# Optimization experiments

Measured on AMD Instinct MI355X. Metric: run time of the kernel, lower is better.

The kernel has to match this reference:

```python
import jax, jax.numpy as jnp
import numpy as np

B, N, H, E, OBS, A, AFF, EFF = 2, 50000, 64, 1_000_000, 128, 18, 512, 256


def setup_inputs() -> dict:
    key = jax.random.key(0)
    ks = jax.random.split(key, 20)
    s = 0.05  # small init to keep gates/tanh unsaturated
    return {
        "obs": jax.random.normal(ks[0], (B, OBS), jnp.float32),
        "state": jax.random.normal(ks[1], (B, N, H), jnp.float32) * 0.1,
        "W_in": jax.random.normal(ks[2], (OBS, H), jnp.float32) * s,
        "b_in": jnp.zeros((H,), jnp.float32),
        "W_msg": jax.random.normal(ks[3], (H, H), jnp.float32) * s,
        "W_gate": jax.random.normal(ks[4], (2 * H, H), jnp.float32) * s,
        "b_gate": jnp.zeros((H,), jnp.float32),
        "W_cand": jax.random.normal(ks[5], (2 * H, H), jnp.float32) * s,
        "b_cand": jnp.zeros((H,), jnp.float32),
        "W_dec": jax.random.normal(ks[6], (H, H), jnp.float32) * s,
        "b_dec": jnp.zeros((H,), jnp.float32),
        "W_mean": jax.random.normal(ks[7], (H, A), jnp.float32) * s,
        "b_mean": jnp.zeros((A,), jnp.float32),
        "W_ls": jax.random.normal(ks[8], (H, A), jnp.float32) * s,
        "b_ls": jnp.zeros((A,), jnp.float32),
        "src_index": jax.random.randint(ks[9], (E,), 0, N),
        "dst_index": jax.random.randint(ks[10], (E,), 0, N),
        "afferent_idx": jax.random.randint(ks[11], (AFF,), 0, N),
        "efferent_idx": jax.random.randint(ks[12], (EFF,), 0, N),
    }


def reference(obs, state, W_in, b_in, W_msg, W_gate, b_gate, W_cand, b_cand,
              W_dec, b_dec, W_mean, b_mean, W_ls, b_ls,
              src_index, dst_index, afferent_idx, efferent_idx):
    # inject obs projection into afferent node slots
    projected = obs @ W_in + b_in                                   # [B, H]
    injected = jnp.zeros_like(state).at[:, afferent_idx, :].set(projected[:, None, :])
    # gather-project-scatter message passing over the edge list
    src_msgs = state[:, src_index, :] @ W_msg                       # [B, E, H]
    messages = jnp.zeros_like(state).at[:, dst_index, :].add(src_msgs)
    # GRU-style gated update
    combined = messages + injected
    gate_in = jnp.concatenate([state, combined], axis=-1)           # [B, N, 2H]
    z = jax.nn.sigmoid(gate_in @ W_gate + b_gate)
    cand = jnp.tanh(gate_in @ W_cand + b_cand)
    next_state = (1.0 - z) * state + z * cand
    # mean-pool readout over efferent nodes, then policy heads
    readout = next_state[:, efferent_idx, :].mean(axis=1)           # [B, H]
    decoded = jnp.tanh(readout @ W_dec + b_dec)
    mean = decoded @ W_mean + b_mean
    log_std = jnp.clip(decoded @ W_ls + b_ls, -5.0, 2.0)
    return mean, log_std, next_state
```

## Files before the change

kernel.cpp:

```cpp
#include <hip/hip_runtime.h>
#include <hip/hip_bf16.h>

constexpr int kN   = 50000;
constexpr int kH   = 64;
constexpr int kB   = 2;
constexpr int kE   = 1000000;
constexpr int kObs = 128;
constexpr int kA   = 18;
constexpr int kAff = 512;
constexpr int kEff = 256;
constexpr int kNH  = kN * kH;
constexpr int kOutOff = 2 * kB * kA;
constexpr int kRanges = 8;
constexpr int kNr  = kN / kRanges;
constexpr int kChunks = 64;
constexpr int kEc  = kE / kChunks;
constexpr int kHistB = kRanges * kChunks;
constexpr int kPackBlocks = (kNH + 8191) / 8192;
constexpr int kWprepBlocks = 20;
constexpr int kScanB = (kN + 255) / 256;

typedef __attribute__((ext_vector_type(8))) short short8_t;
typedef __attribute__((ext_vector_type(4))) float f32x4_t;

__device__ __forceinline__ float ldf(const void* p, int i, int f32) {
  if (f32) return ((const float*)p)[i];
  unsigned short u = ((const unsigned short*)p)[i];
  union { unsigned int x; float f; } v; v.x = ((unsigned int)u) << 16; return v.f;
}
__device__ __forceinline__ void stf(void* p, int i, float val, int f32) {
  if (f32) ((float*)p)[i] = val;
  else ((__hip_bfloat16*)p)[i] = __float2bfloat16(val);
}
__device__ __forceinline__ float lo16(unsigned int w) {
  union { unsigned int i; float f; } v; v.i = w << 16; return v.f;
}
__device__ __forceinline__ float hi16(unsigned int w) {
  union { unsigned int i; float f; } v; v.i = w & 0xffff0000u; return v.f;
}
__device__ __forceinline__ float b2f(unsigned short u) {
  union { unsigned int i; float f; } v; v.i = ((unsigned int)u) << 16; return v.f;
}
__device__ __forceinline__ unsigned int f2b(float f) {
  union { float f; unsigned int u; } v; v.f = f;
  unsigned int r = v.u + 0x7fffu + ((v.u >> 16) & 1u);
  return r >> 16;
}
__device__ __forceinline__ float fsig(float x) {
  return __builtin_amdgcn_rcpf(1.f + __expf(-x));
}
__device__ __forceinline__ float ftanh(float x) {
  return 1.f - 2.f * __builtin_amdgcn_rcpf(__expf(2.f * x) + 1.f);
}
__device__ __forceinline__ int detect64(const unsigned short* wprobe, int t) {
  int hits = 0;
  for (int k = 0; k < 4; ++k) {
    unsigned short u = wprobe[(t * 4 + k) * 2];
    int e = (u >> 7) & 0xFF;
    if ((u & 0x7FFFu) != 0 && e >= 108 && e <= 128) hits++;
  }
  for (int off = 32; off; off >>= 1) hits += __shfl_down(hits, off);
  return (hits < 128) ? 1 : 0;
}

extern "C" __global__ __launch_bounds__(1024) void k_prep(
    const unsigned short* __restrict__ wprobe,
    const void* __restrict__ obs,
    const void* __restrict__ W_in,
    const void* __restrict__ b_in,
    const int* __restrict__ aff_idx,
    const int* __restrict__ dst,
    const void* __restrict__ W_msg,
    const void* __restrict__ W_gate,
    const void* __restrict__ W_cand,
    int* __restrict__ dflag,
    int* __restrict__ flags,
    float* __restrict__ projected,
    int* __restrict__ deg_c,
    unsigned short* __restrict__ wt) {
  __shared__ int sdeg[kNr];
  int t = threadIdx.x, b = blockIdx.x;
  if (b == 0) {
    __shared__ int sflag;
    if (t < 64) { int f = detect64(wprobe, t); if (t == 0) { sflag = f; dflag[0] = f; } }
    for (int i = t; i < kN; i += 1024) flags[i] = 0;
    __syncthreads();
    int f32 = sflag;
    if (t < kAff) flags[aff_idx[t]] = 1;
    if (t < kB * kH) {
      int bb = t >> 6, h = t & 63;
      float acc = ldf(b_in, h, f32);
      for (int o = 0; o < kObs; ++o)
        acc += ldf(obs, bb * kObs + o, f32) * ldf(W_in, o * kH + h, f32);
      projected[t] = acc;
    }
  } else if (b <= kHistB) {
    int h = b - 1, r = h & 7, c = h >> 3;
    int r0 = r * kNr;
    for (int i = t; i < kNr; i += 1024) sdeg[i] = 0;
    __syncthreads();
    int end = (c + 1) * kEc;
    for (int e = c * kEc + t; e < end; e += 1024) {
      unsigned rel = (unsigned)(dst[e] - r0);
      if (rel < (unsigned)kNr) atomicAdd(&sdeg[rel], 1);
    }
    __syncthreads();
    for (int i = t; i < kNr; i += 1024) deg_c[c * kN + r0 + i] = sdeg[i];
  } else {
    __shared__ int sflag;
    if (t < 64) { int f = detect64(wprobe, t); if (t == 0) sflag = f; }
    __syncthreads();
    int f32 = sflag;
    int i = (b - 1 - kHistB) * 1024 + t;
    if (i < 4096) {
      int n = i >> 6, k = i & 63;
      wt[i] = (unsigned short)f2b(ldf(W_msg, k * 64 + n, f32));
    } else if (i < 12288) {
      int j = i - 4096; int n = j >> 7, k = j & 127;
      wt[i] = (unsigned short)f2b(ldf(W_gate, k * 64 + n, f32));
    } else if (i < 20480) {
      int j = i - 12288; int n = j >> 7, k = j & 127;
      wt[i] = (unsigned short)f2b(ldf(W_cand, k * 64 + n, f32));
    }
  }
}

extern "C" __global__ void k_scan1(const int* __restrict__ deg_c,
                                   int* __restrict__ row_off,
                                   int* __restrict__ partials) {
  __shared__ int sd[256];
  int t = threadIdx.x;
  int n = blockIdx.x * 256 + t;
  int s = 0;
  if (n < kN) {
    for (int c = 0; c < kChunks; ++c) s += deg_c[c * kN + n];
  }
  sd[t] = s;
  __syncthreads();
  for (int off = 1; off < 256; off <<= 1) {
    int v = (t >= off) ? sd[t - off] : 0;
    __syncthreads();
    sd[t] += v;
    __syncthreads();
  }
  int excl = sd[t] - s;
  if (t == 255) partials[blockIdx.x] = sd[255];
  if (n < kN) row_off[n] = excl;
}

extern "C" __global__ void k_scan3(int* __restrict__ row_off,
                                   const int* __restrict__ partials,
                                   int* __restrict__ deg_c) {
  __shared__ int sd[256];
  int t = threadIdx.x;
  int s = 0;
  for (int j = t; j < (int)blockIdx.x; j += 256) s += partials[j];
  sd[t] = s;
  __syncthreads();
  for (int off = 128; off; off >>= 1) {
    if (t < off) sd[t] += sd[t + off];
    __syncthreads();
  }
  int base = sd[0];
  int n = blockIdx.x * 256 + t;
  if (n < kN) {
    int v = row_off[n] + base;
    row_off[n] = v;
    int run = v;
#pragma unroll 8
    for (int c = 0; c < kChunks; ++c) {
      int d = deg_c[c * kN + n];
      deg_c[c * kN + n] = run;
      run += d;
    }
  }
  if (blockIdx.x == 0 && t == 0) row_off[kN] = kE;
}

extern "C" __global__ __launch_bounds__(1024) void k_scatter(
    const int* __restrict__ src,
    const int* __restrict__ dst,
    const int* __restrict__ chunk_base,
    int* __restrict__ sorted_src,
    const unsigned short* __restrict__ wprobe,
    const void* __restrict__ state,
    unsigned int* __restrict__ pack) {
  __shared__ int scur[kNr];
  int t = threadIdx.x;
  if (blockIdx.x < kHistB) {
    int r = blockIdx.x & 7, c = blockIdx.x >> 3;
    int r0 = r * kNr;
    for (int i = t; i < kNr; i += 1024) scur[i] = chunk_base[c * kN + r0 + i];
    __syncthreads();
    int end = (c + 1) * kEc;
    for (int e = c * kEc + t; e < end; e += 1024) {
      unsigned rel = (unsigned)(dst[e] - r0);
      if (rel < (unsigned)kNr) {
        int pos = atomicAdd(&scur[rel], 1);
        sorted_src[pos] = src[e];
      }
    }
  } else {
    __shared__ int sflag;
    if (t < 64) { int f = detect64(wprobe, t); if (t == 0) sflag = f; }
    __syncthreads();
    int f32 = sflag;
    int i = (blockIdx.x - kHistB) * 8192 + t * 8;
    if (i < kNH) {
      uint4 o0, o1;
      if (!f32) {
        uint4 a = *(const uint4*)((const unsigned short*)state + i);
        uint4 c4 = *(const uint4*)((const unsigned short*)state + kNH + i);
        o0.x = (a.x & 0xffffu) | (c4.x << 16);
        o0.y = (a.x >> 16)     | (c4.x & 0xffff0000u);
        o0.z = (a.y & 0xffffu) | (c4.y << 16);
        o0.w = (a.y >> 16)     | (c4.y & 0xffff0000u);
        o1.x = (a.z & 0xffffu) | (c4.z << 16);
        o1.y = (a.z >> 16)     | (c4.z & 0xffff0000u);
        o1.z = (a.w & 0xffffu) | (c4.w << 16);
        o1.w = (a.w >> 16)     | (c4.w & 0xffff0000u);
      } else {
        const float* sf = (const float*)state;
        unsigned int w[8];
#pragma unroll
        for (int k = 0; k < 8; ++k)
          w[k] = f2b(sf[i + k]) | (f2b(sf[kNH + i + k]) << 16);
        o0 = make_uint4(w[0], w[1], w[2], w[3]);
        o1 = make_uint4(w[4], w[5], w[6], w[7]);
      }
      *(uint4*)&pack[i] = o0;
      *(uint4*)&pack[i + 4] = o1;
    }
  }
}

extern "C" __global__ __launch_bounds__(256) void k_gather(
    const unsigned int* __restrict__ pack,
    const int* __restrict__ row_off,
    const int* __restrict__ sorted_src,
    unsigned int* __restrict__ agg) {
  int wave = threadIdx.x >> 6, lane = threadIdx.x & 63;
  int n = blockIdx.x * 4 + wave;
  if (n >= kN) return;
  int s  = row_off[n];
  int en = row_off[n + 1];
  int g = lane >> 4, col = lane & 15;
  const uint4* pk4 = (const uint4*)pack;
  float a0x = 0.f, a0y = 0.f, a0z = 0.f, a0w = 0.f;
  float a1x = 0.f, a1y = 0.f, a1z = 0.f, a1w = 0.f;
  for (int e = s; e < en; e += 8) {
#pragma unroll
    for (int h = 0; h < 2; ++h) {
      int ee = e + h * 4 + g;
      int idx = sorted_src[min(ee, en - 1)];
      uint4 wv = pk4[idx * 16 + col];
      if (ee >= en) { wv.x = 0u; wv.y = 0u; wv.z = 0u; wv.w = 0u; }
      a0x += lo16(wv.x); a1x += hi16(wv.x);
      a0y += lo16(wv.y); a1y += hi16(wv.y);
      a0z += lo16(wv.z); a1z += hi16(wv.z);
      a0w += lo16(wv.w); a1w += hi16(wv.w);
    }
  }
  a0x += __shfl_xor(a0x, 16); a0x += __shfl_xor(a0x, 32);
  a0y += __shfl_xor(a0y, 16); a0y += __shfl_xor(a0y, 32);
  a0z += __shfl_xor(a0z, 16); a0z += __shfl_xor(a0z, 32);
  a0w += __shfl_xor(a0w, 16); a0w += __shfl_xor(a0w, 32);
  a1x += __shfl_xor(a1x, 16); a1x += __shfl_xor(a1x, 32);
  a1y += __shfl_xor(a1y, 16); a1y += __shfl_xor(a1y, 32);
  a1z += __shfl_xor(a1z, 16); a1z += __shfl_xor(a1z, 32);
  a1w += __shfl_xor(a1w, 16); a1w += __shfl_xor(a1w, 32);
  if (g == 0) {
    uint4 o;
    o.x = f2b(a0x) | (f2b(a1x) << 16);
    o.y = f2b(a0y) | (f2b(a1y) << 16);
    o.z = f2b(a0z) | (f2b(a1z) << 16);
    o.w = f2b(a0w) | (f2b(a1w) << 16);
    ((uint4*)agg)[n * 16 + col] = o;
  }
}

extern "C" __global__ __launch_bounds__(256) void k_update(
    const unsigned int* __restrict__ pk,
    const unsigned short* __restrict__ wt,
    const void* __restrict__ b_gate,
    const void* __restrict__ b_cand,
    const unsigned int* __restrict__ agg,
    const int* __restrict__ flags,
    const float* __restrict__ projected,
    const int* __restrict__ dflag,
    void* __restrict__ out) {
  __shared__ uint4 lx4[1088];
  unsigned short* lx = (unsigned short*)lx4;
  int f32 = dflag[0];
  int t = threadIdx.x;
  int w = t >> 6, lane = t & 63;
  int q = lane >> 4, l15 = lane & 15;
  int rowb = w * 16;
  int nd0 = blockIdx.x * 32;
  int ndw = nd0 + w * 8;

  const uint4* pk4 = (const uint4*)pk;
  const uint4* ag4 = (const uint4*)agg;
  for (int j = lane; j < 128; j += 64) {
    int ndl = j >> 4, c4 = j & 15;
    int ndg = min(ndw + ndl, kN - 1);
    uint4 pv = pk4[ndg * 16 + c4];
    uint4 av = ag4[ndg * 16 + c4];
    int r0 = rowb + 2 * ndl;
    *(uint2*)&lx[r0 * 136 + c4 * 4] =
        make_uint2((pv.x & 0xffffu) | (pv.y << 16), (pv.z & 0xffffu) | (pv.w << 16));
    *(uint2*)&lx[(r0 + 1) * 136 + c4 * 4] =
        make_uint2((pv.x >> 16) | (pv.y & 0xffff0000u), (pv.z >> 16) | (pv.w & 0xffff0000u));
    *(uint2*)&lx[r0 * 136 + 64 + c4 * 4] =
        make_uint2((av.x & 0xffffu) | (av.y << 16), (av.z & 0xffffu) | (av.w << 16));
    *(uint2*)&lx[(r0 + 1) * 136 + 64 + c4 * 4] =
        make_uint2((av.x >> 16) | (av.y & 0xffff0000u), (av.z >> 16) | (av.w & 0xffff0000u));
  }

  const unsigned short* wm = wt;
  const unsigned short* wg = wt + 4096;
  const unsigned short* wc = wt + 12288;

  short8_t a0 = *(const short8_t*)&lx[(rowb + l15) * 136 + 64 + q * 8];
  short8_t a1 = *(const short8_t*)&lx[(rowb + l15) * 136 + 96 + q * 8];
  f32x4_t msgc[4];
#pragma unroll
  for (int ct = 0; ct < 4; ++ct) {
    f32x4_t acc = {0.f, 0.f, 0.f, 0.f};
    short8_t b0 = *(const short8_t*)&wm[(ct * 16 + l15) * 64 + q * 8];
    short8_t b1 = *(const short8_t*)&wm[(ct * 16 + l15) * 64 + 32 + q * 8];
    acc = __builtin_amdgcn_mfma_f32_16x16x32_bf16(a0, b0, acc, 0, 0, 0);
    acc = __builtin_amdgcn_mfma_f32_16x16x32_bf16(a1, b1, acc, 0, 0, 0);
    msgc[ct] = acc;
  }
  int nA = ndw + q * 2, nB = nA + 1;
  int flA = (nA < kN) ? flags[nA] : 0;
  int flB = (nB < kN) ? flags[nB] : 0;
#pragma unroll
  for (int ct = 0; ct < 4; ++ct) {
    int col = ct * 16 + l15;
    float pj0 = projected[col], pj1 = projected[64 + col];
#pragma unroll
    for (int r = 0; r < 4; ++r) {
      int row = rowb + q * 4 + r;
      int fl = (r < 2) ? flA : flB;
      float inj = fl ? ((row & 1) ? pj1 : pj0) : 0.f;
      lx[row * 136 + 64 + col] = (unsigned short)f2b(msgc[ct][r] + inj);
    }
  }

  short8_t xa[4];
#pragma unroll
  for (int ks = 0; ks < 4; ++ks)
    xa[ks] = *(const short8_t*)&lx[(rowb + l15) * 136 + ks * 32 + q * 8];
  float ps[16];
#pragma unroll
  for (int ct = 0; ct < 4; ++ct)
#pragma unroll
    for (int rp = 0; rp < 2; ++rp) {
      int row = rowb + q * 4 + 2 * rp;
      ps[ct * 4 + rp * 2 + 0] = b2f(lx[row * 136 + ct * 16 + l15]);
      ps[ct * 4 + rp * 2 + 1] = b2f(lx[(row + 1) * 136 + ct * 16 + l15]);
    }
  float* soutw = (float*)((char*)lx4 + w * 4352);
#pragma unroll
  for (int ct = 0; ct < 4; ++ct) {
    f32x4_t accg = {0.f, 0.f, 0.f, 0.f}, accc = {0.f, 0.f, 0.f, 0.f};
#pragma unroll
    for (int ks = 0; ks < 4; ++ks) {
      short8_t bg = *(const short8_t*)&wg[(ct * 16 + l15) * 128 + ks * 32 + q * 8];
      short8_t bc = *(const short8_t*)&wc[(ct * 16 + l15) * 128 + ks * 32 + q * 8];
      accg = __builtin_amdgcn_mfma_f32_16x16x32_bf16(xa[ks], bg, accg, 0, 0, 0);
      accc = __builtin_amdgcn_mfma_f32_16x16x32_bf16(xa[ks], bc, accc, 0, 0, 0);
    }
    int col = ct * 16 + l15;
    float bgv = ldf(b_gate, col, f32), bcv = ldf(b_cand, col, f32);
#pragma unroll
    for (int rp = 0; rp < 2; ++rp) {
      int r = q * 4 + 2 * rp;
      float z0 = fsig(accg[2 * rp] + bgv);
      float c0 = ftanh(accc[2 * rp] + bcv);
      soutw[r * 64 + col] = (1.f - z0) * ps[ct * 4 + rp * 2 + 0] + z0 * c0;
      float z1 = fsig(accg[2 * rp + 1] + bgv);
      float c1 = ftanh(accc[2 * rp + 1] + bcv);
      soutw[(r + 1) * 64 + col] = (1.f - z1) * ps[ct * 4 + rp * 2 + 1] + z1 * c1;
    }
  }
  __syncthreads();

  int nvalid = min(32, kN - nd0) * 64;
  if (f32) {
    float* po = (float*)out + kOutOff;
#pragma unroll
    for (int p = 0; p < 2; ++p)
      for (int j = t * 4; j < nvalid; j += 1024) {
        int ndl = j >> 6, c = j & 63;
        int wv = ndl >> 3, r = ((ndl & 7) << 1) + p;
        float4 v = *(float4*)((char*)lx4 + wv * 4352 + r * 256 + c * 4);
        *(float4*)(po + p * kNH + nd0 * 64 + j) = v;
      }
  } else {
    unsigned short* po = (unsigned short*)out + kOutOff;
#pragma unroll
    for (int p = 0; p < 2; ++p)
      for (int j = t * 8; j < nvalid; j += 2048) {
        int ndl = j >> 6, c = j & 63;
        int wv = ndl >> 3, r = ((ndl & 7) << 1) + p;
        const char* base = (const char*)lx4 + wv * 4352 + r * 256 + c * 4;
        float4 v0 = *(const float4*)base;
        float4 v1 = *(const float4*)(base + 16);
        uint4 o;
        o.x = f2b(v0.x) | (f2b(v0.y) << 16);
        o.y = f2b(v0.z) | (f2b(v0.w) << 16);
        o.z = f2b(v1.x) | (f2b(v1.y) << 16);
        o.w = f2b(v1.z) | (f2b(v1.w) << 16);
        *(uint4*)(po + p * kNH + nd0 * 64 + j) = o;
      }
  }
}

extern "C" __global__ void k_readout(const void* __restrict__ W_dec,
                                     const void* __restrict__ b_dec,
                                     const void* __restrict__ W_mean,
                                     const void* __restrict__ b_mean,
                                     const void* __restrict__ W_ls,
                                     const void* __restrict__ b_ls,
                                     const int* __restrict__ eff_idx,
                                     const int* __restrict__ dflag,
                                     void* __restrict__ out) {
  __shared__ float part[8][64];
  __shared__ float ro[128], dec[128];
  int f32 = dflag[0];
  int t = threadIdx.x;
  int wv = t >> 6, lane = t & 63;
  int b = wv >> 2, g = wv & 3;
  float acc = 0.f;
#pragma unroll 4
  for (int i = 0; i < 64; ++i) {
    int n = eff_idx[g * 64 + i];
    acc += ldf(out, kOutOff + b * kNH + n * 64 + lane, f32);
  }
  part[wv][lane] = acc;
  __syncthreads();
  if (t < 128) {
    int bb = t >> 6, h = t & 63;
    float s = part[bb * 4 + 0][h] + part[bb * 4 + 1][h] +
              part[bb * 4 + 2][h] + part[bb * 4 + 3][h];
    ro[t] = s * (1.f / kEff);
  }
  __syncthreads();
  if (t < 128) {
    int bb = t >> 6, h = t & 63;
    float d = ldf(b_dec, h, f32);
    for (int k = 0; k < 64; ++k) d += ro[bb * 64 + k] * ldf(W_dec, k * 64 + h, f32);
    dec[t] = tanhf(d);
  }
  __syncthreads();
  if (t < kB * kA) {
    int bb = t / kA, a = t % kA;
    float m = ldf(b_mean, a, f32), l = ldf(b_ls, a, f32);
    for (int k = 0; k < 64; ++k) {
      float dv = dec[bb * 64 + k];
      m += dv * ldf(W_mean, k * kA + a, f32);
      l += dv * ldf(W_ls, k * kA + a, f32);
    }
    l = fminf(fmaxf(l, -5.f), 2.f);
    stf(out, t, m, f32);
    stf(out, kB * kA + t, l, f32);
  }
}

extern "C" void kernel_launch(void* const* d_in, const int* in_sizes, int n_in,
                              void* d_out, int out_size, void* d_ws, size_t ws_size,
                              hipStream_t stream) {
  (void)in_sizes; (void)n_in; (void)out_size; (void)ws_size;
  const void* obs    = d_in[0];
  const void* state  = d_in[1];
  const void* W_in   = d_in[2];
  const void* b_in   = d_in[3];
  const void* W_msg  = d_in[4];
  const void* W_gate = d_in[5];
  const void* b_gate = d_in[6];
  const void* W_cand = d_in[7];
  const void* b_cand = d_in[8];
  const void* W_dec  = d_in[9];
  const void* b_dec  = d_in[10];
  const void* W_mean = d_in[11];
  const void* b_mean = d_in[12];
  const void* W_ls   = d_in[13];
  const void* b_ls   = d_in[14];
  const int* src = (const int*)d_in[15];
  const int* dst = (const int*)d_in[16];
  const int* aff = (const int*)d_in[17];
  const int* eff = (const int*)d_in[18];

  int* wsp        = (int*)d_ws;
  int* flags      = wsp;
  int* deg_c      = flags + kN;
  int* row_off    = deg_c + kChunks * kN;
  int* partials   = row_off + (kN + 64);
  int* dflag      = partials + 512;
  float* projected = (float*)(dflag + 16);
  int* sorted_src  = (int*)(projected + 128);
  unsigned int* pk  = (unsigned int*)(sorted_src + kE);
  unsigned int* agg = pk + kNH;
  unsigned short* wt = (unsigned short*)(agg + kNH);

  k_prep<<<1 + kHistB + kWprepBlocks, 1024, 0, stream>>>(
      (const unsigned short*)W_cand, obs, W_in, b_in, aff, dst,
      W_msg, W_gate, W_cand, dflag, flags, projected, deg_c, wt);
  k_scan1<<<kScanB, 256, 0, stream>>>(deg_c, row_off, partials);
  k_scan3<<<kScanB, 256, 0, stream>>>(row_off, partials, deg_c);
  k_scatter<<<kHistB + kPackBlocks, 1024, 0, stream>>>(
      src, dst, deg_c, sorted_src, (const unsigned short*)W_cand, state, pk);
  k_gather<<<(kN + 3) / 4, 256, 0, stream>>>(pk, row_off, sorted_src, agg);
  k_update<<<(kN + 31) / 32, 256, 0, stream>>>(pk, wt, b_gate, b_cand,
                                               agg, flags, projected, dflag, d_out);
  k_readout<<<1, 512, 0, stream>>>(W_dec, b_dec, W_mean, b_mean, W_ls, b_ls, eff,
                                   dflag, d_out);
}
```

Before: 285.1 us.

## Fuse readout into update via last-block atomic accumulation; swizzle gather block order

```diff
diff --git a/kernel.cpp b/kernel.cpp
--- a/kernel.cpp
+++ b/kernel.cpp
@@ -19,6 +19,8 @@
 constexpr int kPackBlocks = (kNH + 8191) / 8192;
 constexpr int kWprepBlocks = 20;
 constexpr int kScanB = (kN + 255) / 256;
+constexpr int kGatB = kRanges * 1563;
+constexpr int kUpdB = (kN + 31) / 32;
 
 typedef __attribute__((ext_vector_type(8))) short short8_t;
 typedef __attribute__((ext_vector_type(4))) float f32x4_t;
@@ -77,13 +79,17 @@
     int* __restrict__ flags,
     float* __restrict__ projected,
     int* __restrict__ deg_c,
-    unsigned short* __restrict__ wt) {
+    unsigned short* __restrict__ wt,
+    float* __restrict__ eff_acc,
+    int* __restrict__ ucount) {
   __shared__ int sdeg[kNr];
   int t = threadIdx.x, b = blockIdx.x;
   if (b == 0) {
     __shared__ int sflag;
     if (t < 64) { int f = detect64(wprobe, t); if (t == 0) { sflag = f; dflag[0] = f; } }
     for (int i = t; i < kN; i += 1024) flags[i] = 0;
+    if (t < 128) eff_acc[t] = 0.f;
+    if (t == 128) ucount[0] = 0;
     __syncthreads();
     int f32 = sflag;
     if (t < kAff) flags[aff_idx[t]] = 1;
@@ -240,8 +246,10 @@
     const int* __restrict__ sorted_src,
     unsigned int* __restrict__ agg) {
   int wave = threadIdx.x >> 6, lane = threadIdx.x & 63;
-  int n = blockIdx.x * 4 + wave;
-  if (n >= kN) return;
+  int x = blockIdx.x & 7, j = blockIdx.x >> 3;
+  int local = j * 4 + wave;
+  if (local >= kNr) return;
+  int n = x * kNr + local;
   int s  = row_off[n];
   int en = row_off[n + 1];
   int g = lane >> 4, col = lane & 15;
@@ -288,8 +296,19 @@
     const int* __restrict__ flags,
     const float* __restrict__ projected,
     const int* __restrict__ dflag,
-    void* __restrict__ out) {
+    void* __restrict__ out,
+    const void* __restrict__ W_dec,
+    const void* __restrict__ b_dec,
+    const void* __restrict__ W_mean,
+    const void* __restrict__ b_mean,
+    const void* __restrict__ W_ls,
+    const void* __restrict__ b_ls,
+    const int* __restrict__ eff_idx,
+    float* __restrict__ eff_acc,
+    int* __restrict__ ucount) {
   __shared__ uint4 lx4[1088];
+  __shared__ int smatch[256];
+  __shared__ int smcnt, slast;
   unsigned short* lx = (unsigned short*)lx4;
   int f32 = dflag[0];
   int t = threadIdx.x;
@@ -298,6 +317,7 @@
   int rowb = w * 16;
   int nd0 = blockIdx.x * 32;
   int ndw = nd0 + w * 8;
+  if (t == 0) smcnt = 0;
 
   const uint4* pk4 = (const uint4*)pk;
   const uint4* ag4 = (const uint4*)agg;
@@ -388,6 +408,12 @@
   }
   __syncthreads();
 
+  if (t < kEff) {
+    unsigned rel = (unsigned)(eff_idx[t] - nd0);
+    if (rel < 32u) { int s = atomicAdd(&smcnt, 1); smatch[s] = (int)rel; }
+  }
+  __syncthreads();
+
   int nvalid = min(32, kN - nd0) * 64;
   if (f32) {
     float* po = (float*)out + kOutOff;
@@ -417,37 +443,31 @@
         *(uint4*)(po + p * kNH + nd0 * 64 + j) = o;
       }
   }
-}
-
-extern "C" __global__ void k_readout(const void* __restrict__ W_dec,
-                                     const void* __restrict__ b_dec,
-                                     const void* __restrict__ W_mean,
-                                     const void* __restrict__ b_mean,
-                                     const void* __restrict__ W_ls,
-                                     const void* __restrict__ b_ls,
-                                     const int* __restrict__ eff_idx,
-                                     const int* __restrict__ dflag,
-                                     void* __restrict__ out) {
-  __shared__ float part[8][64];
-  __shared__ float ro[128], dec[128];
-  int f32 = dflag[0];
-  int t = threadIdx.x;
-  int wv = t >> 6, lane = t & 63;
-  int b = wv >> 2, g = wv & 3;
-  float acc = 0.f;
-#pragma unroll 4
-  for (int i = 0; i < 64; ++i) {
-    int n = eff_idx[g * 64 + i];
-    acc += ldf(out, kOutOff + b * kNH + n * 64 + lane, f32);
-  }
-  part[wv][lane] = acc;
-  __syncthreads();
-  if (t < 128) {
-    int bb = t >> 6, h = t & 63;
-    float s = part[bb * 4 + 0][h] + part[bb * 4 + 1][h] +
-              part[bb * 4 + 2][h] + part[bb * 4 + 3][h];
-    ro[t] = s * (1.f / kEff);
-  }
+
+  int cnt = smcnt;
+  for (int m = 0; m < cnt; ++m) {
+    int rel = smatch[m];
+    if (t < 128) {
+      int p = t >> 6, c = t & 63;
+      int wv = rel >> 3, r = ((rel & 7) << 1) + p;
+      float v = *(const float*)((const char*)lx4 + wv * 4352 + r * 256 + c * 4);
+      if (!f32) v = b2f((unsigned short)f2b(v));
+      atomicAdd(&eff_acc[p * 64 + c], v);
+    }
+  }
+  __syncthreads();
+  if (t == 0) {
+    __threadfence();
+    slast = (atomicAdd(ucount, 1) == kUpdB - 1) ? 1 : 0;
+  }
+  __syncthreads();
+  if (!slast) return;
+
+  float* ro  = (float*)lx4;
+  float* dec = ro + 128;
+  if (t < 128)
+    ro[t] = __hip_atomic_load(&eff_acc[t], __ATOMIC_RELAXED,
+                              __HIP_MEMORY_SCOPE_AGENT) * (1.f / kEff);
   __syncthreads();
   if (t < 128) {
     int bb = t >> 6, h = t & 63;
@@ -501,21 +521,24 @@
   int* partials   = row_off + (kN + 64);
   int* dflag      = partials + 512;
   float* projected = (float*)(dflag + 16);
-  int* sorted_src  = (int*)(projected + 128);
+  float* eff_acc   = projected + 128;
+  int* ucount      = (int*)(eff_acc + 128);
+  int* sorted_src  = ucount + 64;
   unsigned int* pk  = (unsigned int*)(sorted_src + kE);
   unsigned int* agg = pk + kNH;
   unsigned short* wt = (unsigned short*)(agg + kNH);
 
   k_prep<<<1 + kHistB + kWprepBlocks, 1024, 0, stream>>>(
       (const unsigned short*)W_cand, obs, W_in, b_in, aff, dst,
-      W_msg, W_gate, W_cand, dflag, flags, projected, deg_c, wt);
+      W_msg, W_gate, W_cand, dflag, flags, projected, deg_c, wt,
+      eff_acc, ucount);
   k_scan1<<<kScanB, 256, 0, stream>>>(deg_c, row_off, partials);
   k_scan3<<<kScanB, 256, 0, stream>>>(row_off, partials, deg_c);
   k_scatter<<<kHistB + kPackBlocks, 1024, 0, stream>>>(
       src, dst, deg_c, sorted_src, (const unsigned short*)W_cand, state, pk);
-  k_gather<<<(kN + 3) / 4, 256, 0, stream>>>(pk, row_off, sorted_src, agg);
-  k_update<<<(kN + 31) / 32, 256, 0, stream>>>(pk, wt, b_gate, b_cand,
-                                               agg, flags, projected, dflag, d_out);
-  k_readout<<<1, 512, 0, stream>>>(W_dec, b_dec, W_mean, b_mean, W_ls, b_ls, eff,
-                                   dflag, d_out);
-}
+  k_gather<<<kGatB, 256, 0, stream>>>(pk, row_off, sorted_src, agg);
+  k_update<<<kUpdB, 256, 0, stream>>>(pk, wt, b_gate, b_cand,
+                                      agg, flags, projected, dflag, d_out,
+                                      W_dec, b_dec, W_mean, b_mean, W_ls, b_ls,
+                                      eff, eff_acc, ucount);
+}
```

Result: slower. 305.1 us (+7.0%).
